# Kernel optimization log

Hardware: AMD Instinct MI355X
Metric: run time of the kernel (lower is better)

Reference implementation:

```python
import jax, jax.numpy as jnp
import numpy as np

N = 10000      # nodes
E = 1_000_000  # edges (avg degree 100)
T = 6          # time steps (states.size(0)); T-1 recurrent steps
HID = 32       # hidden_feats, forced by M out=32 and U in=2*hid


def _linear(key, fan_in, fan_out):
    k1, k2 = jax.random.split(key)
    s = 1.0 / np.sqrt(fan_in)
    w = jax.random.uniform(k1, (fan_in, fan_out), minval=-s, maxval=s, dtype=jnp.float32)
    b = jax.random.uniform(k2, (fan_out,), minval=-s, maxval=s, dtype=jnp.float32)
    return w, b


def setup_inputs() -> dict:
    key = jax.random.key(0)
    ks = jax.random.split(key, 12)
    states = jax.random.normal(ks[0], (T, N), dtype=jnp.float32)
    priority = jax.random.uniform(ks[1], (N,), dtype=jnp.float32)
    edges_mat = jax.random.normal(ks[2], (N, N), dtype=jnp.float32) * 0.1
    src = jax.random.randint(ks[3], (E,), 0, N)
    # dst constructed so every node has at least one incoming edge (segment_max well-defined)
    dst = jnp.arange(E, dtype=jnp.int32) % N
    enc_w, enc_b = _linear(ks[4], 1 + HID + 1, HID)   # encoder: in_feats + hidden + 1
    M_w, M_b = _linear(ks[5], 2 * HID + 1, HID)        # M: 2*hidden + edge_feats -> 32
    U_w, U_b = _linear(ks[6], 2 * HID, HID)
    dn_w, dn_b = _linear(ks[7], 2 * HID, 1)            # decoder_nextnode
    du_w, du_b = _linear(ks[8], 2 * HID + 1, 1)        # decoder_update
    term_w, term_b = _linear(ks[9], HID, 1)
    return dict(states=states, priority=priority, edges_mat=edges_mat, src=src, dst=dst,
                enc_w=enc_w, enc_b=enc_b, M_w=M_w, M_b=M_b, U_w=U_w, U_b=U_b,
                dn_w=dn_w, dn_b=dn_b, du_w=du_w, du_b=du_b, term_w=term_w, term_b=term_b)


def reference(states, priority, edges_mat, src, dst,
              enc_w, enc_b, M_w, M_b, U_w, U_b,
              dn_w, dn_b, du_w, du_b, term_w, term_b):
    n = states.shape[1]
    t = states.shape[0]
    edge_feat = edges_mat[src, dst]  # (E,) gather like edges_mat[graph.edges()]
    pri = priority[:, None]          # (N,1)

    def step(carry, _):
        state, hidden = carry                                   # (N,), (N,HID)
        inp = jnp.concatenate([state[:, None], hidden, pri], 1)  # (N, 1+HID+1)
        z = inp @ enc_w + enc_b                                  # (N, HID)
        m_in = jnp.concatenate([z[src], z[dst], edge_feat[:, None]], 1)  # (E, 2*HID+1)
        msg = m_in @ M_w + M_b                                   # (E, HID)
        u_input = jax.ops.segment_max(msg, dst, num_segments=n)  # max-reduce into dst mailboxes
        new_hidden = jnp.concatenate([z, u_input], 1) @ U_w + U_b  # (N, HID)
        h_mean = jnp.mean(new_hidden, axis=0, keepdims=True)
        loc = jnp.concatenate([new_hidden, h_mean], 0) @ term_w + term_b  # (N+1, 1)
        stop = jnp.max(jax.nn.sigmoid(loc))
        nne = jnp.concatenate([new_hidden, z], 1) @ dn_w + dn_b   # (N,1)
        new_state = (jnp.concatenate([new_hidden, z, nne], 1) @ du_w + du_b)[:, 0]  # (N,)
        return (new_state, new_hidden), (new_state, stop, nne[:, 0])

    hidden0 = jnp.zeros((n, HID), dtype=states.dtype)
    _, (new_states, stops, nnes) = jax.lax.scan(step, (states[0], hidden0), None, length=t - 1)

    preds = jnp.concatenate([states[0:1], new_states], 0)                 # (T, N)
    preds_stop = jnp.concatenate([jnp.zeros((1,), preds.dtype), stops])[None, :, None]  # (1, T, 1)
    preds_nextnode = nnes.T[:, :, None]                                   # (N, T-1, 1)
    return preds, preds_stop, preds_nextnode
```

## Files before the change

kernel.cpp:

```cpp
#include <hip/hip_runtime.h>
#include <hip/hip_cooperative_groups.h>
#include <math.h>

namespace cg = cooperative_groups;

#define NN 10000
#define EE 1000000
#define HIDN 32
#define NSTEP 5
#define GROUPS 8
#define NBLK (NN / GROUPS)
#define NTHR 256

#define STOP_OFF (6*NN)
#define PN_OFF   (6*NN + 6)

__device__ __forceinline__ unsigned fkey(float f) {
  unsigned u = __float_as_uint(f);
  return (u & 0x80000000u) ? ~u : (u | 0x80000000u);
}
__device__ __forceinline__ float fkey_dec(unsigned k) {
  unsigned u = (k & 0x80000000u) ? (k ^ 0x80000000u) : ~k;
  return __uint_as_float(u);
}

__global__ __launch_bounds__(NTHR, 5) void k_all(
    const float* __restrict__ states, const float* __restrict__ pri,
    const float* __restrict__ edges_mat, const int* __restrict__ src,
    const float* __restrict__ enc_w, const float* __restrict__ enc_b,
    const float* __restrict__ M_w, const float* __restrict__ M_b,
    const float* __restrict__ U_w, const float* __restrict__ U_b,
    const float* __restrict__ dn_w, const float* __restrict__ dn_b,
    const float* __restrict__ du_w, const float* __restrict__ du_b,
    const float* __restrict__ term_w, const float* __restrict__ term_b,
    int2* __restrict__ se, float* __restrict__ Abuf,
    float* __restrict__ hsum, unsigned* __restrict__ locmax,
    float* __restrict__ d_out)
{
  __shared__ float s_ew[34 * 32];
  __shared__ float s_ms[1024], s_md[1024], s_uwz[1024], s_uwu[1024];
  __shared__ float s_eb[32], s_mb[32], s_ub[32];
  __shared__ float s_zr[GROUPS][32], s_ur[GROUPS][32], s_nh[GROUPS][32];
  __shared__ float s_loc[GROUPS];

  const int tid = threadIdx.x;
  const int g = tid >> 5, o = tid & 31;
  const int j = blockIdx.x * GROUPS + g;
  const int gid = blockIdx.x * NTHR + tid;

  for (int e = gid; e < EE; e += NBLK * NTHR) {
    int s = src[e];
    int d = e % NN;
    float ef = edges_mat[(size_t)s * NN + d];
    se[e] = make_int2(s, __float_as_int(ef));
  }
  for (int x = gid; x < NN; x += NBLK * NTHR) d_out[x] = states[x];
  if (gid < 64) hsum[gid] = 0.f;
  if (gid == 0) { locmax[0] = 0u; locmax[1] = 0u; d_out[STOP_OFF] = 0.f; }

  for (int i = tid; i < 34 * 32; i += NTHR) s_ew[i] = enc_w[i];
  for (int i = tid; i < 1024; i += NTHR) {
    s_ms[i]  = M_w[i];        s_md[i]  = M_w[1024 + i];
    s_uwz[i] = U_w[i];        s_uwu[i] = U_w[1024 + i];
  }
  if (tid < 32) { s_eb[tid] = enc_b[tid]; s_mb[tid] = M_b[tid]; s_ub[tid] = U_b[tid]; }
  __syncthreads();

  const float pr   = pri[j];
  const float mw64 = M_w[64 * 32 + o];
  const float twv  = term_w[o];
  const float dnw0 = dn_w[o], dnw1 = dn_w[32 + o];
  const float duw0 = du_w[o], duw1 = du_w[32 + o];
  const float du64 = du_w[64], dnb0 = dn_b[0], dub0 = du_b[0];

  {
    float st = states[j];
    float zv = s_eb[o] + st * s_ew[o] + pr * s_ew[33 * 32 + o];
    s_zr[g][o] = zv;
    __syncthreads();
    float av = 0.f, bv = s_mb[o];
    #pragma unroll
    for (int i = 0; i < 32; i++) {
      float zi = s_zr[g][i];
      av = fmaf(zi, s_ms[i * 32 + o], av);
      bv = fmaf(zi, s_md[i * 32 + o], bv);
    }
    Abuf[(j << 5) | o] = av;
    s_nh[g][o] = 0.f;
    __syncthreads();
    s_zr[g][o] = zv;
    __syncthreads();
    float z_init = zv, b_init = bv;
    __shared__ float s_dummy; (void)s_dummy;
    cg::this_grid().sync();

    float z_reg = z_init, base_reg = b_init;

    for (int t = 0; t < NSTEP; t++) {
      if (blockIdx.x == 0 && t > 0 && tid < 32) {
        int pb = (t - 1) & 1;
        float v = hsum[pb * 32 + tid] * (1.0f / NN) * twv;
        #pragma unroll
        for (int m = 16; m >= 1; m >>= 1) v += __shfl_xor(v, m, 32);
        if (tid == 0) {
          float mx = fmaxf(fkey_dec(locmax[pb]), v);
          d_out[STOP_OFF + t] = 1.f / (1.f + expf(-(mx + term_b[0])));
          locmax[pb] = 0u;
        }
        hsum[pb * 32 + tid] = 0.f;
      }

      const float* __restrict__ Ar = Abuf + (size_t)(t & 1) * (NN * HIDN);
      float red0 = -3.4e38f, red1 = -3.4e38f;
      {
        const int2* sep = se + j;
        #pragma unroll 2
        for (int kb = 0; kb < 100; kb += 10) {
          int2 v[10];
          #pragma unroll
          for (int q = 0; q < 10; q++) v[q] = sep[(kb + q) * NN];
          #pragma unroll
          for (int q = 0; q < 10; q++) {
            float a = Ar[(v[q].x << 5) | o];
            float m = fmaf(__int_as_float(v[q].y), mw64, a);
            if (q & 1) red1 = fmaxf(red1, m); else red0 = fmaxf(red0, m);
          }
        }
      }
      float u_o = fmaxf(red0, red1) + base_reg;

      s_zr[g][o] = z_reg; s_ur[g][o] = u_o;
      __syncthreads();
      float nh = s_ub[o];
      #pragma unroll
      for (int i = 0; i < 32; i++) {
        nh = fmaf(s_zr[g][i], s_uwz[i * 32 + o], nh);
        nh = fmaf(s_ur[g][i], s_uwu[i * 32 + o], nh);
      }

      float lv  = nh * twv;
      float dnv = nh * dnw0 + z_reg * dnw1;
      float duv = nh * duw0 + z_reg * duw1;
      #pragma unroll
      for (int m = 16; m >= 1; m >>= 1) {
        lv  += __shfl_xor(lv,  m, 32);
        dnv += __shfl_xor(dnv, m, 32);
        duv += __shfl_xor(duv, m, 32);
      }
      float nne = dnv + dnb0;
      float ns  = duv + nne * du64 + dub0;
      if (o == 0) {
        d_out[(t + 1) * NN + j]      = ns;
        d_out[PN_OFF + j * NSTEP + t] = nne;
        s_loc[g] = lv;
      }
      s_nh[g][o] = nh;
      __syncthreads();
      if (tid < 32) {
        float hp = 0.f;
        #pragma unroll
        for (int gg = 0; gg < GROUPS; gg++) hp += s_nh[gg][tid];
        atomicAdd(&hsum[(t & 1) * 32 + tid], hp);
      }
      if (tid == 0) {
        float m = s_loc[0];
        #pragma unroll
        for (int gg = 1; gg < GROUPS; gg++) m = fmaxf(m, s_loc[gg]);
        atomicMax(&locmax[t & 1], fkey(m));
      }

      if (t < NSTEP - 1) {
        float z2 = s_eb[o] + ns * s_ew[o] + pr * s_ew[33 * 32 + o];
        #pragma unroll
        for (int i = 0; i < 32; i++) z2 = fmaf(s_nh[g][i], s_ew[(1 + i) * 32 + o], z2);
        __syncthreads();
        s_zr[g][o] = z2;
        __syncthreads();
        float av2 = 0.f, bv2 = s_mb[o];
        #pragma unroll
        for (int i = 0; i < 32; i++) {
          float zi = s_zr[g][i];
          av2 = fmaf(zi, s_ms[i * 32 + o], av2);
          bv2 = fmaf(zi, s_md[i * 32 + o], bv2);
        }
        float* __restrict__ Aw = Abuf + (size_t)((t + 1) & 1) * (NN * HIDN);
        Aw[(j << 5) | o] = av2;
        z_reg = z2; base_reg = bv2;
      }

      cg::this_grid().sync();
    }

    if (blockIdx.x == 0 && tid < 32) {
      float v = hsum[tid] * (1.0f / NN) * twv;
      #pragma unroll
      for (int m = 16; m >= 1; m >>= 1) v += __shfl_xor(v, m, 32);
      if (tid == 0) {
        float mx = fmaxf(fkey_dec(locmax[0]), v);
        d_out[STOP_OFF + NSTEP] = 1.f / (1.f + expf(-(mx + term_b[0])));
      }
    }
  }
}

__global__ __launch_bounds__(256) void k_pre(
    const int* __restrict__ src,
    const float* __restrict__ edges_mat, const float* __restrict__ states,
    int2* __restrict__ se, float* __restrict__ hidden, float* __restrict__ d_out,
    float* __restrict__ hsum, unsigned* __restrict__ locmax)
{
  int i = blockIdx.x * blockDim.x + threadIdx.x;
  int stride = blockDim.x * gridDim.x;
  for (int e = i; e < EE; e += stride) {
    int s = src[e];
    int d = e % NN;
    float ef = edges_mat[(size_t)s * NN + d];
    se[e] = make_int2(s, __float_as_int(ef));
  }
  for (int x = i; x < NN * HIDN; x += stride) hidden[x] = 0.f;
  for (int x = i; x < NN; x += stride) d_out[x] = states[x];
  if (i == 0) { d_out[STOP_OFF] = 0.f; *locmax = 0u; }
  if (i >= 256 && i < 256 + 32) hsum[i - 256] = 0.f;
}

__global__ __launch_bounds__(256) void k_znode(
    const float* __restrict__ state, const float* __restrict__ pri,
    const float* __restrict__ hidden,
    const float* __restrict__ enc_w, const float* __restrict__ enc_b,
    const float* __restrict__ M_w, const float* __restrict__ M_b,
    const float* __restrict__ term_w, const float* __restrict__ term_b,
    float* __restrict__ z, float* __restrict__ A, float* __restrict__ base,
    float* __restrict__ hsum, unsigned* __restrict__ locmax,
    float* __restrict__ d_out, int t)
{
  __shared__ float s_ew[34 * 32], s_eb[32], s_ms[32 * 32], s_md[32 * 32], s_mb[32];
  __shared__ float s_h[GROUPS][32], s_z[GROUPS][32];
  int tid = threadIdx.x;
  for (int i = tid; i < 34 * 32; i += 256) s_ew[i] = enc_w[i];
  for (int i = tid; i < 32 * 32; i += 256) { s_ms[i] = M_w[i]; s_md[i] = M_w[32 * 32 + i]; }
  if (tid < 32) { s_eb[tid] = enc_b[tid]; s_mb[tid] = M_b[tid]; }

  if (blockIdx.x == 0 && t > 0 && tid < 32) {
    float v = hsum[tid] * (1.0f / NN) * term_w[tid];
    #pragma unroll
    for (int m = 16; m >= 1; m >>= 1) v += __shfl_xor(v, m, 32);
    if (tid == 0) {
      float mx = fmaxf(fkey_dec(*locmax), v);
      d_out[STOP_OFF + t] = 1.f / (1.f + expf(-(mx + term_b[0])));
      *locmax = 0u;
    }
    hsum[tid] = 0.f;
  }

  int g = tid >> 5, o = tid & 31;
  int j = blockIdx.x * GROUPS + g;
  s_h[g][o] = hidden[(j << 5) | o];
  __syncthreads();
  float st = state[j], pr = pri[j];
  float zv = s_eb[o] + st * s_ew[o] + pr * s_ew[33 * 32 + o];
  #pragma unroll
  for (int i = 0; i < 32; i++) zv = fmaf(s_h[g][i], s_ew[(1 + i) * 32 + o], zv);
  s_z[g][o] = zv;
  z[(j << 5) | o] = zv;
  __syncthreads();
  float av = 0.f, bv = s_mb[o];
  #pragma unroll
  for (int i = 0; i < 32; i++) {
    float zi = s_z[g][i];
    av = fmaf(zi, s_ms[i * 32 + o], av);
    bv = fmaf(zi, s_md[i * 32 + o], bv);
  }
  A[(j << 5) | o] = av;
  base[(j << 5) | o] = bv;
}

__global__ __launch_bounds__(256) void k_edge(
    const int2* __restrict__ se,
    const float* __restrict__ z, const float* __restrict__ A,
    const float* __restrict__ base,
    const float* __restrict__ U_w, const float* __restrict__ U_b,
    const float* __restrict__ dn_w, const float* __restrict__ dn_b,
    const float* __restrict__ du_w, const float* __restrict__ du_b,
    const float* __restrict__ term_w, const float* __restrict__ M_w,
    float* __restrict__ hidden, float* __restrict__ d_out,
    float* __restrict__ hsum, unsigned* __restrict__ locmax, int t)
{
  __shared__ float s_uwz[32 * 32], s_uwu[32 * 32], s_ub[32];
  __shared__ float s_zr[GROUPS][32], s_ur[GROUPS][32], s_nh[GROUPS][32];
  __shared__ float s_loc[GROUPS];
  int tid = threadIdx.x;
  for (int i = tid; i < 32 * 32; i += 256) { s_uwz[i] = U_w[i]; s_uwu[i] = U_w[32 * 32 + i]; }
  if (tid < 32) s_ub[tid] = U_b[tid];
  int g = tid >> 5, o = tid & 31;
  int j = blockIdx.x * GROUPS + g;
  float mw64 = M_w[64 * 32 + o];

  float red = -3.4e38f;
  #pragma unroll 4
  for (int k = 0; k < 100; k++) {
    int2 v = se[j + k * NN];
    float a = A[(v.x << 5) | o];
    red = fmaxf(red, fmaf(__int_as_float(v.y), mw64, a));
  }
  float u_o = red + base[(j << 5) | o];
  float z_o = z[(j << 5) | o];
  s_zr[g][o] = z_o; s_ur[g][o] = u_o;
  __syncthreads();
  float nh = s_ub[o];
  #pragma unroll
  for (int i = 0; i < 32; i++) {
    nh = fmaf(s_zr[g][i], s_uwz[i * 32 + o], nh);
    nh = fmaf(s_ur[g][i], s_uwu[i * 32 + o], nh);
  }
  hidden[(j << 5) | o] = nh;

  float lv  = nh * term_w[o];
  float dnv = nh * dn_w[o] + z_o * dn_w[32 + o];
  float duv = nh * du_w[o] + z_o * du_w[32 + o];
  #pragma unroll
  for (int m = 16; m >= 1; m >>= 1) {
    lv  += __shfl_xor(lv,  m, 32);
    dnv += __shfl_xor(dnv, m, 32);
    duv += __shfl_xor(duv, m, 32);
  }
  if (o == 0) {
    float nne = dnv + dn_b[0];
    float nsv = duv + nne * du_w[64] + du_b[0];
    d_out[(t + 1) * NN + j] = nsv;
    d_out[PN_OFF + j * NSTEP + t] = nne;
    s_loc[g] = lv;
  }
  s_nh[g][o] = nh;
  __syncthreads();
  if (tid < 32) {
    float hp = 0.f;
    #pragma unroll
    for (int gg = 0; gg < GROUPS; gg++) hp += s_nh[gg][tid];
    atomicAdd(&hsum[tid], hp);
  }
  if (tid == 0) {
    float m = s_loc[0];
    #pragma unroll
    for (int gg = 1; gg < GROUPS; gg++) m = fmaxf(m, s_loc[gg]);
    atomicMax(locmax, fkey(m));
  }
}

__global__ void k_stop(const float* __restrict__ hsum, const unsigned* __restrict__ locmax,
                       const float* __restrict__ term_w, const float* __restrict__ term_b,
                       float* __restrict__ d_out, int t)
{
  int o = threadIdx.x;
  float v = (o < 32) ? (hsum[o] * (1.0f / NN)) * term_w[o] : 0.f;
  #pragma unroll
  for (int m = 16; m >= 1; m >>= 1) v += __shfl_xor(v, m, 32);
  if (o == 0) {
    float mx = fmaxf(fkey_dec(*locmax), v);
    float x = mx + term_b[0];
    d_out[STOP_OFF + 1 + t] = 1.f / (1.f + expf(-x));
  }
}

extern "C" void kernel_launch(void* const* d_in, const int* in_sizes, int n_in,
                              void* d_out_v, int out_size, void* d_ws, size_t ws_size,
                              hipStream_t stream)
{
  const float* states = (const float*)d_in[0];
  const float* pri    = (const float*)d_in[1];
  const float* edges  = (const float*)d_in[2];
  const int*   src    = (const int*)d_in[3];
  const float* enc_w  = (const float*)d_in[5];
  const float* enc_b  = (const float*)d_in[6];
  const float* M_w    = (const float*)d_in[7];
  const float* M_b    = (const float*)d_in[8];
  const float* U_w    = (const float*)d_in[9];
  const float* U_b    = (const float*)d_in[10];
  const float* dn_w   = (const float*)d_in[11];
  const float* dn_b   = (const float*)d_in[12];
  const float* du_w   = (const float*)d_in[13];
  const float* du_b   = (const float*)d_in[14];
  const float* term_w = (const float*)d_in[15];
  const float* term_b = (const float*)d_in[16];
  float* out = (float*)d_out_v;
  float* ws = (float*)d_ws;

  static int coop_ok = -1;
  if (coop_ok < 0) {
    int nb = 0;
    hipError_t e1 = hipOccupancyMaxActiveBlocksPerMultiprocessor(&nb, k_all, NTHR, 0);
    hipDeviceProp_t prop;
    int dev = 0;
    hipGetDevice(&dev);
    hipError_t e2 = hipGetDeviceProperties(&prop, dev);
    coop_ok = (e1 == hipSuccess && e2 == hipSuccess &&
               prop.cooperativeLaunch &&
               (long)nb * prop.multiProcessorCount >= NBLK) ? 1 : 0;
  }

  if (coop_ok == 1) {
    int2*  se     = (int2*)ws;
    float* Abuf   = ws + 2 * EE;
    float* hsum   = Abuf + 2 * NN * HIDN;
    unsigned* locmax = (unsigned*)(hsum + 64);

    void* args[] = {
      (void*)&states, (void*)&pri, (void*)&edges, (void*)&src,
      (void*)&enc_w, (void*)&enc_b, (void*)&M_w, (void*)&M_b,
      (void*)&U_w, (void*)&U_b, (void*)&dn_w, (void*)&dn_b,
      (void*)&du_w, (void*)&du_b, (void*)&term_w, (void*)&term_b,
      (void*)&se, (void*)&Abuf, (void*)&hsum, (void*)&locmax, (void*)&out
    };
    hipLaunchCooperativeKernel((void*)k_all, dim3(NBLK), dim3(NTHR), args, 0, stream);
    return;
  }

  int2*  se     = (int2*)ws;
  float* z      = ws + 2 * EE;
  float* Abuf   = z + NN * HIDN;
  float* base   = Abuf + NN * HIDN;
  float* hidden = base + NN * HIDN;
  float* hsum   = hidden + NN * HIDN;
  unsigned* locmax = (unsigned*)(hsum + 32);

  hipLaunchKernelGGL(k_pre, dim3(4096), dim3(256), 0, stream,
                     src, edges, states, se, hidden, out, hsum, locmax);
  for (int t = 0; t < NSTEP; t++) {
    const float* state = out + t * NN;
    hipLaunchKernelGGL(k_znode, dim3(NN / GROUPS), dim3(256), 0, stream,
                       state, pri, hidden, enc_w, enc_b, M_w, M_b, term_w, term_b,
                       z, Abuf, base, hsum, locmax, out, t);
    hipLaunchKernelGGL(k_edge, dim3(NN / GROUPS), dim3(256), 0, stream,
                       se, z, Abuf, base, U_w, U_b, dn_w, dn_b, du_w, du_b,
                       term_w, M_w, hidden, out, hsum, locmax, t);
  }
  hipLaunchKernelGGL(k_stop, dim3(1), dim3(64), 0, stream,
                     hsum, locmax, term_w, term_b, out, NSTEP - 1);
}
```

Measured before the change: 796.5 us.

## Replace random edge-matrix gather with row-streamed CSR scatter and multi-kernel pipeline

Removes the cooperative single-kernel path. The random 4-byte gather from the 400MB edges_mat is replaced by a histogram, scan and scatter over src rows, followed by a kernel that streams each needed row into LDS and writes edge features into a block-contiguous layout. The edge kernel now stages its block's source offsets and edge features in shared memory before the A gather. This trades several extra preprocessing kernels, atomics and launches for coalesced reads of edges_mat, and gives up the grid-sync persistent kernel.

Result: slower. 954.9 us (+19.9%).

```diff
diff --git a/kernel.cpp b/kernel.cpp
--- a/kernel.cpp
+++ b/kernel.cpp
@@ -1,8 +1,5 @@
 #include <hip/hip_runtime.h>
-#include <hip/hip_cooperative_groups.h>
 #include <math.h>
-
-namespace cg = cooperative_groups;
 
 #define NN 10000
 #define EE 1000000
@@ -11,6 +8,8 @@
 #define GROUPS 8
 #define NBLK (NN / GROUPS)
 #define NTHR 256
+#define DEG 100
+#define CPAD 16
 
 #define STOP_OFF (6*NN)
 #define PN_OFF   (6*NN + 6)
@@ -24,203 +23,89 @@
   return __uint_as_float(u);
 }
 
-__global__ __launch_bounds__(NTHR, 5) void k_all(
-    const float* __restrict__ states, const float* __restrict__ pri,
-    const float* __restrict__ edges_mat, const int* __restrict__ src,
-    const float* __restrict__ enc_w, const float* __restrict__ enc_b,
-    const float* __restrict__ M_w, const float* __restrict__ M_b,
-    const float* __restrict__ U_w, const float* __restrict__ U_b,
-    const float* __restrict__ dn_w, const float* __restrict__ dn_b,
-    const float* __restrict__ du_w, const float* __restrict__ du_b,
-    const float* __restrict__ term_w, const float* __restrict__ term_b,
-    int2* __restrict__ se, float* __restrict__ Abuf,
-    float* __restrict__ hsum, unsigned* __restrict__ locmax,
-    float* __restrict__ d_out)
-{
-  __shared__ float s_ew[34 * 32];
-  __shared__ float s_ms[1024], s_md[1024], s_uwz[1024], s_uwu[1024];
-  __shared__ float s_eb[32], s_mb[32], s_ub[32];
-  __shared__ float s_zr[GROUPS][32], s_ur[GROUPS][32], s_nh[GROUPS][32];
-  __shared__ float s_loc[GROUPS];
-
-  const int tid = threadIdx.x;
-  const int g = tid >> 5, o = tid & 31;
-  const int j = blockIdx.x * GROUPS + g;
-  const int gid = blockIdx.x * NTHR + tid;
-
-  for (int e = gid; e < EE; e += NBLK * NTHR) {
-    int s = src[e];
-    int d = e % NN;
-    float ef = edges_mat[(size_t)s * NN + d];
-    se[e] = make_int2(s, __float_as_int(ef));
-  }
-  for (int x = gid; x < NN; x += NBLK * NTHR) d_out[x] = states[x];
-  if (gid < 64) hsum[gid] = 0.f;
-  if (gid == 0) { locmax[0] = 0u; locmax[1] = 0u; d_out[STOP_OFF] = 0.f; }
-
-  for (int i = tid; i < 34 * 32; i += NTHR) s_ew[i] = enc_w[i];
-  for (int i = tid; i < 1024; i += NTHR) {
-    s_ms[i]  = M_w[i];        s_md[i]  = M_w[1024 + i];
-    s_uwz[i] = U_w[i];        s_uwu[i] = U_w[1024 + i];
-  }
-  if (tid < 32) { s_eb[tid] = enc_b[tid]; s_mb[tid] = M_b[tid]; s_ub[tid] = U_b[tid]; }
-  __syncthreads();
-
-  const float pr   = pri[j];
-  const float mw64 = M_w[64 * 32 + o];
-  const float twv  = term_w[o];
-  const float dnw0 = dn_w[o], dnw1 = dn_w[32 + o];
-  const float duw0 = du_w[o], duw1 = du_w[32 + o];
-  const float du64 = du_w[64], dnb0 = dn_b[0], dub0 = du_b[0];
-
-  {
-    float st = states[j];
-    float zv = s_eb[o] + st * s_ew[o] + pr * s_ew[33 * 32 + o];
-    s_zr[g][o] = zv;
-    __syncthreads();
-    float av = 0.f, bv = s_mb[o];
-    #pragma unroll
-    for (int i = 0; i < 32; i++) {
-      float zi = s_zr[g][i];
-      av = fmaf(zi, s_ms[i * 32 + o], av);
-      bv = fmaf(zi, s_md[i * 32 + o], bv);
-    }
-    Abuf[(j << 5) | o] = av;
-    s_nh[g][o] = 0.f;
-    __syncthreads();
-    s_zr[g][o] = zv;
-    __syncthreads();
-    float z_init = zv, b_init = bv;
-    __shared__ float s_dummy; (void)s_dummy;
-    cg::this_grid().sync();
-
-    float z_reg = z_init, base_reg = b_init;
-
-    for (int t = 0; t < NSTEP; t++) {
-      if (blockIdx.x == 0 && t > 0 && tid < 32) {
-        int pb = (t - 1) & 1;
-        float v = hsum[pb * 32 + tid] * (1.0f / NN) * twv;
-        #pragma unroll
-        for (int m = 16; m >= 1; m >>= 1) v += __shfl_xor(v, m, 32);
-        if (tid == 0) {
-          float mx = fmaxf(fkey_dec(locmax[pb]), v);
-          d_out[STOP_OFF + t] = 1.f / (1.f + expf(-(mx + term_b[0])));
-          locmax[pb] = 0u;
-        }
-        hsum[pb * 32 + tid] = 0.f;
-      }
-
-      const float* __restrict__ Ar = Abuf + (size_t)(t & 1) * (NN * HIDN);
-      float red0 = -3.4e38f, red1 = -3.4e38f;
-      {
-        const int2* sep = se + j;
-        #pragma unroll 2
-        for (int kb = 0; kb < 100; kb += 10) {
-          int2 v[10];
-          #pragma unroll
-          for (int q = 0; q < 10; q++) v[q] = sep[(kb + q) * NN];
-          #pragma unroll
-          for (int q = 0; q < 10; q++) {
-            float a = Ar[(v[q].x << 5) | o];
-            float m = fmaf(__int_as_float(v[q].y), mw64, a);
-            if (q & 1) red1 = fmaxf(red1, m); else red0 = fmaxf(red0, m);
-          }
-        }
-      }
-      float u_o = fmaxf(red0, red1) + base_reg;
-
-      s_zr[g][o] = z_reg; s_ur[g][o] = u_o;
-      __syncthreads();
-      float nh = s_ub[o];
-      #pragma unroll
-      for (int i = 0; i < 32; i++) {
-        nh = fmaf(s_zr[g][i], s_uwz[i * 32 + o], nh);
-        nh = fmaf(s_ur[g][i], s_uwu[i * 32 + o], nh);
-      }
-
-      float lv  = nh * twv;
-      float dnv = nh * dnw0 + z_reg * dnw1;
-      float duv = nh * duw0 + z_reg * duw1;
-      #pragma unroll
-      for (int m = 16; m >= 1; m >>= 1) {
-        lv  += __shfl_xor(lv,  m, 32);
-        dnv += __shfl_xor(dnv, m, 32);
-        duv += __shfl_xor(duv, m, 32);
-      }
-      float nne = dnv + dnb0;
-      float ns  = duv + nne * du64 + dub0;
-      if (o == 0) {
-        d_out[(t + 1) * NN + j]      = ns;
-        d_out[PN_OFF + j * NSTEP + t] = nne;
-        s_loc[g] = lv;
-      }
-      s_nh[g][o] = nh;
-      __syncthreads();
-      if (tid < 32) {
-        float hp = 0.f;
-        #pragma unroll
-        for (int gg = 0; gg < GROUPS; gg++) hp += s_nh[gg][tid];
-        atomicAdd(&hsum[(t & 1) * 32 + tid], hp);
-      }
-      if (tid == 0) {
-        float m = s_loc[0];
-        #pragma unroll
-        for (int gg = 1; gg < GROUPS; gg++) m = fmaxf(m, s_loc[gg]);
-        atomicMax(&locmax[t & 1], fkey(m));
-      }
-
-      if (t < NSTEP - 1) {
-        float z2 = s_eb[o] + ns * s_ew[o] + pr * s_ew[33 * 32 + o];
-        #pragma unroll
-        for (int i = 0; i < 32; i++) z2 = fmaf(s_nh[g][i], s_ew[(1 + i) * 32 + o], z2);
-        __syncthreads();
-        s_zr[g][o] = z2;
-        __syncthreads();
-        float av2 = 0.f, bv2 = s_mb[o];
-        #pragma unroll
-        for (int i = 0; i < 32; i++) {
-          float zi = s_zr[g][i];
-          av2 = fmaf(zi, s_ms[i * 32 + o], av2);
-          bv2 = fmaf(zi, s_md[i * 32 + o], bv2);
-        }
-        float* __restrict__ Aw = Abuf + (size_t)((t + 1) & 1) * (NN * HIDN);
-        Aw[(j << 5) | o] = av2;
-        z_reg = z2; base_reg = bv2;
-      }
-
-      cg::this_grid().sync();
-    }
-
-    if (blockIdx.x == 0 && tid < 32) {
-      float v = hsum[tid] * (1.0f / NN) * twv;
-      #pragma unroll
-      for (int m = 16; m >= 1; m >>= 1) v += __shfl_xor(v, m, 32);
-      if (tid == 0) {
-        float mx = fmaxf(fkey_dec(locmax[0]), v);
-        d_out[STOP_OFF + NSTEP] = 1.f / (1.f + expf(-(mx + term_b[0])));
-      }
-    }
-  }
-}
-
-__global__ __launch_bounds__(256) void k_pre(
-    const int* __restrict__ src,
-    const float* __restrict__ edges_mat, const float* __restrict__ states,
-    int2* __restrict__ se, float* __restrict__ hidden, float* __restrict__ d_out,
-    float* __restrict__ hsum, unsigned* __restrict__ locmax)
+__global__ __launch_bounds__(256) void k_zero(
+    unsigned* __restrict__ cnt, unsigned* __restrict__ cnt2,
+    float* __restrict__ hidden, const float* __restrict__ states,
+    float* __restrict__ d_out, float* __restrict__ hsum,
+    unsigned* __restrict__ locmax)
+{
+  int i = blockIdx.x * blockDim.x + threadIdx.x;
+  int stride = blockDim.x * gridDim.x;
+  for (int x = i; x < NN * CPAD; x += stride) { cnt[x] = 0u; cnt2[x] = 0u; }
+  for (int x = i; x < NN * HIDN; x += stride) hidden[x] = 0.f;
+  for (int x = i; x < NN; x += stride) d_out[x] = states[x];
+  if (i == 0) { d_out[STOP_OFF] = 0.f; *locmax = 0u; }
+  if (i >= 256 && i < 256 + 32) hsum[i - 256] = 0.f;
+}
+
+__global__ __launch_bounds__(256) void k_hist(const int* __restrict__ src,
+                                              unsigned* __restrict__ cnt)
+{
+  int i = blockIdx.x * blockDim.x + threadIdx.x;
+  int stride = blockDim.x * gridDim.x;
+  for (int e = i; e < EE; e += stride)
+    atomicAdd(&cnt[src[e] * CPAD], 1u);
+}
+
+__global__ __launch_bounds__(256) void k_scan(const unsigned* __restrict__ cnt,
+                                              unsigned* __restrict__ sbase)
+{
+  __shared__ unsigned s_part[256];
+  int tid = threadIdx.x;
+  int s0 = tid * 40, s1 = (s0 + 40 < NN) ? s0 + 40 : NN;
+  unsigned mysum = 0;
+  for (int s = s0; s < s1; s++) mysum += cnt[s * CPAD];
+  s_part[tid] = mysum;
+  __syncthreads();
+  if (tid == 0) {
+    unsigned run = 0;
+    for (int i = 0; i < 256; i++) { unsigned t = s_part[i]; s_part[i] = run; run += t; }
+  }
+  __syncthreads();
+  unsigned run = s_part[tid];
+  for (int s = s0; s < s1; s++) { sbase[s] = run; run += cnt[s * CPAD]; }
+  if (tid == 255) sbase[NN] = EE;
+}
+
+__global__ __launch_bounds__(256) void k_scatter(const int* __restrict__ src,
+                                                 const unsigned* __restrict__ sbase,
+                                                 unsigned* __restrict__ cnt2,
+                                                 unsigned* __restrict__ rowlist)
 {
   int i = blockIdx.x * blockDim.x + threadIdx.x;
   int stride = blockDim.x * gridDim.x;
   for (int e = i; e < EE; e += stride) {
     int s = src[e];
-    int d = e % NN;
-    float ef = edges_mat[(size_t)s * NN + d];
-    se[e] = make_int2(s, __float_as_int(ef));
-  }
-  for (int x = i; x < NN * HIDN; x += stride) hidden[x] = 0.f;
-  for (int x = i; x < NN; x += stride) d_out[x] = states[x];
-  if (i == 0) { d_out[STOP_OFF] = 0.f; *locmax = 0u; }
-  if (i >= 256 && i < 256 + 32) hsum[i - 256] = 0.f;
+    int d = e % NN, kk = e / NN;
+    unsigned dest = (unsigned)((d >> 3) * 800 + kk * 8 + (d & 7));
+    unsigned pos = sbase[s] + atomicAdd(&cnt2[s * CPAD], 1u);
+    rowlist[pos] = dest;
+  }
+}
+
+__global__ __launch_bounds__(256) void k_stream(const float* __restrict__ edges_mat,
+                                                const unsigned* __restrict__ sbase,
+                                                const unsigned* __restrict__ rowlist,
+                                                int2* __restrict__ se2)
+{
+  __shared__ __align__(16) float s_row[NN];
+  int tid = threadIdx.x;
+  #pragma unroll 1
+  for (int r = 0; r < 4; r++) {
+    int s = blockIdx.x * 4 + r;
+    const float4* rp = (const float4*)(edges_mat + (size_t)s * NN);
+    for (int i = tid; i < NN / 4; i += NTHR)
+      ((float4*)s_row)[i] = rp[i];
+    __syncthreads();
+    unsigned cb = sbase[s], ce = sbase[s + 1];
+    int sshift = s << 5;
+    for (unsigned i = cb + tid; i < ce; i += NTHR) {
+      unsigned dest = rowlist[i];
+      int d = (int)(dest / 800u) * 8 + (int)(dest & 7u);
+      se2[dest] = make_int2(sshift, __float_as_int(s_row[d]));
+    }
+    __syncthreads();
+  }
 }
 
 __global__ __launch_bounds__(256) void k_znode(
@@ -229,7 +114,7 @@
     const float* __restrict__ enc_w, const float* __restrict__ enc_b,
     const float* __restrict__ M_w, const float* __restrict__ M_b,
     const float* __restrict__ term_w, const float* __restrict__ term_b,
-    float* __restrict__ z, float* __restrict__ A, float* __restrict__ base,
+    float* __restrict__ z, float* __restrict__ A, float* __restrict__ ubase,
     float* __restrict__ hsum, unsigned* __restrict__ locmax,
     float* __restrict__ d_out, int t)
 {
@@ -271,13 +156,13 @@
     bv = fmaf(zi, s_md[i * 32 + o], bv);
   }
   A[(j << 5) | o] = av;
-  base[(j << 5) | o] = bv;
-}
-
-__global__ __launch_bounds__(256) void k_edge(
-    const int2* __restrict__ se,
+  ubase[(j << 5) | o] = bv;
+}
+
+__global__ __launch_bounds__(256, 4) void k_edge(
+    const int2* __restrict__ se2,
     const float* __restrict__ z, const float* __restrict__ A,
-    const float* __restrict__ base,
+    const float* __restrict__ ubase,
     const float* __restrict__ U_w, const float* __restrict__ U_b,
     const float* __restrict__ dn_w, const float* __restrict__ dn_b,
     const float* __restrict__ du_w, const float* __restrict__ du_b,
@@ -288,21 +173,42 @@
   __shared__ float s_uwz[32 * 32], s_uwu[32 * 32], s_ub[32];
   __shared__ float s_zr[GROUPS][32], s_ur[GROUPS][32], s_nh[GROUPS][32];
   __shared__ float s_loc[GROUPS];
+  __shared__ int   s_so[GROUPS][DEG];
+  __shared__ float s_ef[GROUPS][DEG];
   int tid = threadIdx.x;
   for (int i = tid; i < 32 * 32; i += 256) { s_uwz[i] = U_w[i]; s_uwu[i] = U_w[32 * 32 + i]; }
   if (tid < 32) s_ub[tid] = U_b[tid];
+
+  #pragma unroll
+  for (int i = 0; i < 4; i++) {
+    int idx = tid + i * NTHR;
+    if (idx < GROUPS * DEG) {
+      int2 v = se2[blockIdx.x * (GROUPS * DEG) + idx];
+      int gg = idx & 7, kk = idx >> 3;
+      s_so[gg][kk] = v.x;
+      s_ef[gg][kk] = __int_as_float(v.y);
+    }
+  }
   int g = tid >> 5, o = tid & 31;
   int j = blockIdx.x * GROUPS + g;
   float mw64 = M_w[64 * 32 + o];
-
-  float red = -3.4e38f;
-  #pragma unroll 4
-  for (int k = 0; k < 100; k++) {
-    int2 v = se[j + k * NN];
-    float a = A[(v.x << 5) | o];
-    red = fmaxf(red, fmaf(__int_as_float(v.y), mw64, a));
-  }
-  float u_o = red + base[(j << 5) | o];
+  __syncthreads();
+
+  float red0 = -3.4e38f, red1 = -3.4e38f;
+  #pragma unroll 1
+  for (int kb = 0; kb < DEG; kb += 20) {
+    int off[20]; float av[20];
+    #pragma unroll
+    for (int q = 0; q < 20; q++) off[q] = s_so[g][kb + q] | o;
+    #pragma unroll
+    for (int q = 0; q < 20; q++) av[q] = A[off[q]];
+    #pragma unroll
+    for (int q = 0; q < 20; q++) {
+      float m = fmaf(s_ef[g][kb + q], mw64, av[q]);
+      if (q & 1) red1 = fmaxf(red1, m); else red0 = fmaxf(red0, m);
+    }
+  }
+  float u_o = fmaxf(red0, red1) + ubase[(j << 5) | o];
   float z_o = z[(j << 5) | o];
   s_zr[g][o] = z_o; s_ur[g][o] = u_o;
   __syncthreads();
@@ -384,53 +290,32 @@
   float* out = (float*)d_out_v;
   float* ws = (float*)d_ws;
 
-  static int coop_ok = -1;
-  if (coop_ok < 0) {
-    int nb = 0;
-    hipError_t e1 = hipOccupancyMaxActiveBlocksPerMultiprocessor(&nb, k_all, NTHR, 0);
-    hipDeviceProp_t prop;
-    int dev = 0;
-    hipGetDevice(&dev);
-    hipError_t e2 = hipGetDeviceProperties(&prop, dev);
-    coop_ok = (e1 == hipSuccess && e2 == hipSuccess &&
-               prop.cooperativeLaunch &&
-               (long)nb * prop.multiProcessorCount >= NBLK) ? 1 : 0;
-  }
-
-  if (coop_ok == 1) {
-    int2*  se     = (int2*)ws;
-    float* Abuf   = ws + 2 * EE;
-    float* hsum   = Abuf + 2 * NN * HIDN;
-    unsigned* locmax = (unsigned*)(hsum + 64);
-
-    void* args[] = {
-      (void*)&states, (void*)&pri, (void*)&edges, (void*)&src,
-      (void*)&enc_w, (void*)&enc_b, (void*)&M_w, (void*)&M_b,
-      (void*)&U_w, (void*)&U_b, (void*)&dn_w, (void*)&dn_b,
-      (void*)&du_w, (void*)&du_b, (void*)&term_w, (void*)&term_b,
-      (void*)&se, (void*)&Abuf, (void*)&hsum, (void*)&locmax, (void*)&out
-    };
-    hipLaunchCooperativeKernel((void*)k_all, dim3(NBLK), dim3(NTHR), args, 0, stream);
-    return;
-  }
-
-  int2*  se     = (int2*)ws;
-  float* z      = ws + 2 * EE;
-  float* Abuf   = z + NN * HIDN;
-  float* base   = Abuf + NN * HIDN;
-  float* hidden = base + NN * HIDN;
-  float* hsum   = hidden + NN * HIDN;
-  unsigned* locmax = (unsigned*)(hsum + 32);
-
-  hipLaunchKernelGGL(k_pre, dim3(4096), dim3(256), 0, stream,
-                     src, edges, states, se, hidden, out, hsum, locmax);
+  int2*     se2     = (int2*)ws;
+  unsigned* rowlist = (unsigned*)(ws + 2 * EE);
+  unsigned* cnt     = rowlist + EE;
+  unsigned* cnt2    = cnt + NN * CPAD;
+  unsigned* sbase   = cnt2 + NN * CPAD;
+  float*    z       = (float*)(sbase + NN + 1);
+  float*    A       = z + NN * HIDN;
+  float*    ubase   = A + NN * HIDN;
+  float*    hidden  = ubase + NN * HIDN;
+  float*    hsum    = hidden + NN * HIDN;
+  unsigned* locmax  = (unsigned*)(hsum + 32);
+
+  hipLaunchKernelGGL(k_zero,    dim3(1024), dim3(256), 0, stream,
+                     cnt, cnt2, hidden, states, out, hsum, locmax);
+  hipLaunchKernelGGL(k_hist,    dim3(1024), dim3(256), 0, stream, src, cnt);
+  hipLaunchKernelGGL(k_scan,    dim3(1),    dim3(256), 0, stream, cnt, sbase);
+  hipLaunchKernelGGL(k_scatter, dim3(1024), dim3(256), 0, stream, src, sbase, cnt2, rowlist);
+  hipLaunchKernelGGL(k_stream,  dim3(2500), dim3(256), 0, stream, edges, sbase, rowlist, se2);
+
   for (int t = 0; t < NSTEP; t++) {
     const float* state = out + t * NN;
-    hipLaunchKernelGGL(k_znode, dim3(NN / GROUPS), dim3(256), 0, stream,
+    hipLaunchKernelGGL(k_znode, dim3(NBLK), dim3(256), 0, stream,
                        state, pri, hidden, enc_w, enc_b, M_w, M_b, term_w, term_b,
-                       z, Abuf, base, hsum, locmax, out, t);
-    hipLaunchKernelGGL(k_edge, dim3(NN / GROUPS), dim3(256), 0, stream,
-                       se, z, Abuf, base, U_w, U_b, dn_w, dn_b, du_w, du_b,
+                       z, A, ubase, hsum, locmax, out, t);
+    hipLaunchKernelGGL(k_edge, dim3(NBLK), dim3(256), 0, stream,
+                       se2, z, A, ubase, U_w, U_b, dn_w, dn_b, du_w, du_b,
                        term_w, M_w, hidden, out, hsum, locmax, t);
   }
   hipLaunchKernelGGL(k_stop, dim3(1), dim3(64), 0, stream,
```
